# Optimization experiments

Hardware: AMD Instinct MI355X
Metric: run time of the kernel (lower is better)

The kernel has to match this reference:

```python
import jax, jax.numpy as jnp
import numpy as np
from jax import lax

# --- STE quantizers matching the torch autograd.Functions ---
@jax.custom_vjp
def binary_quantize_w(x):
    return jnp.sign(x)

def _bqw_fwd(x):
    return jnp.sign(x), None

def _bqw_bwd(_, g):
    return (g,)  # straight-through identity

binary_quantize_w.defvjp(_bqw_fwd, _bqw_bwd)

@jax.custom_vjp
def binary_quantize_a(x):
    return jnp.sign(x)

def _bqa_fwd(x):
    return jnp.sign(x), x

def _bqa_bwd(x, g):
    return (jnp.clip(2.0 - jnp.abs(2.0 * x), a_min=0.0) * g,)

binary_quantize_a.defvjp(_bqa_fwd, _bqa_bwd)

STRIDE = 1
PAD = 1

def setup_inputs() -> dict:
    key = jax.random.key(0)
    k1, k2, k3 = jax.random.split(key, 3)
    x = jax.random.normal(k1, (32, 256, 56, 56), dtype=jnp.float32)
    M = jax.random.normal(k2, (256, 256, 3, 3), dtype=jnp.float32)
    Alpha = jax.random.uniform(k3, (256, 1, 1), dtype=jnp.float32)
    return {"x": x, "M": M, "Alpha": Alpha}

def reference(x, M, Alpha):
    bw = binary_quantize_w(M)        # (O, I, kh, kw), +/-1
    ba = binary_quantize_a(x)        # (N, C, H, W), +/-1
    out = lax.conv_general_dilated(
        ba, bw,
        window_strides=(STRIDE, STRIDE),
        padding=[(PAD, PAD), (PAD, PAD)],
        dimension_numbers=("NCHW", "OIHW", "NCHW"),
    )
    # Alpha (O,1,1) broadcasts over (N, O, H, W) trailing dims -> per-channel scale
    return out * Alpha
```

## Files before the change

kernel.cpp:

```cpp
#include <hip/hip_runtime.h>
#include <stdint.h>


typedef __attribute__((ext_vector_type(16))) float floatx16;
typedef __attribute__((ext_vector_type(8)))  int   intx8;

#define N_IMG 32
#define C_IN  256
#define O_OUT 256
#define HP 58
#define WP 58
#define GPI 3136
#define APAD_POS ((size_t)N_IMG * HP * WP)
#define ROWB 128
#define APAD_BYTES (APAD_POS * ROWB)
#define TPI 13
#define AL_CHUNKS 536
#define WL_CHUNKS 768
#define WROW 8192
#define WPK_STEP (3 * WROW)

__device__ __forceinline__ unsigned int sgn4(float x) {
    return x > 0.f ? 0x2u : (x < 0.f ? 0xAu : 0u);
}

__device__ __forceinline__ void glds16(const unsigned char* g, unsigned char* l) {
    __builtin_amdgcn_global_load_lds(
        (const __attribute__((address_space(1))) unsigned int*)g,
        (__attribute__((address_space(3))) unsigned int*)l, 16, 0, 0);
}

__device__ __forceinline__ unsigned int nib16(unsigned int w) {
    return (w & 0xFu) | ((w >> 4) & 0xF0u) |
           ((w >> 8) & 0xF00u) | ((w >> 12) & 0xF000u);
}
__device__ __forceinline__ unsigned int nibc(unsigned int lo, unsigned int hi) {
    return nib16(lo) | (nib16(hi) << 16);
}

__global__ __launch_bounds__(256) void binarize_act(
    const float* __restrict__ x, unsigned char* __restrict__ apad)
{
    int bid = blockIdx.x;
    int n = bid / HP;
    int hp = bid - n * HP;
    int tid = threadIdx.x;

    unsigned char* rowp = apad + (size_t)(n * HP + hp) * WP * ROWB;
    uint4 z = {0u, 0u, 0u, 0u};

    if (hp == 0 || hp == HP - 1) {
#pragma unroll
        for (int j = 0; j < 2; ++j) {
            int t = tid + 256 * j;
            if (t < WP * 8) {
                int w = t >> 3, g = t & 7;
                *(uint4*)(rowp + (size_t)w * ROWB + g * 16) = z;
            }
        }
        return;
    }
    int h = hp - 1;

    __shared__ unsigned int tile[C_IN * 15];
    __shared__ unsigned int lds2[56 * 65];

    const float* xb = x + ((size_t)n * C_IN) * GPI + h * 56;
#pragma unroll
    for (int j = 0; j < 14; ++j) {
        int t = tid + 256 * j;
        int ci = t / 14;
        int w4 = t - ci * 14;
        float4 v = *(const float4*)(xb + (size_t)ci * GPI + w4 * 4);
        tile[ci * 15 + w4] = sgn4(v.x) | (sgn4(v.y) << 8) |
                             (sgn4(v.z) << 16) | (sgn4(v.w) << 24);
    }
    __syncthreads();

#pragma unroll
    for (int j = 0; j < 14; ++j) {
        int t = tid + 256 * j;
        int wlo = t & 3;
        int cq  = (t >> 2) & 63;
        int whi = t >> 8;
        int sh = wlo * 8;
        unsigned int r = 0;
#pragma unroll
        for (int i = 0; i < 4; ++i) {
            unsigned int v = tile[(cq * 4 + i) * 15 + whi];
            r |= ((v >> sh) & 0xFFu) << (8 * i);
        }
        lds2[(whi * 4 + wlo) * 65 + cq] = r;
    }
    __syncthreads();

#pragma unroll
    for (int j = 0; j < 2; ++j) {
        int t = tid + 256 * j;
        if (t < 448) {
            int w = t >> 3, g = t & 7;
            uint4 a = *(uint4*)&lds2[w * 65 + g * 8];
            uint4 b = *(uint4*)&lds2[w * 65 + g * 8 + 4];
            uint4 v;
            v.x = nibc(a.x, a.y);
            v.y = nibc(a.z, a.w);
            v.z = nibc(b.x, b.y);
            v.w = nibc(b.z, b.w);
            *(uint4*)(rowp + (size_t)(w + 1) * ROWB + g * 16) = v;
        }
    }
    if (tid < 16) {
        int g = tid & 7;
        int col = (tid >> 3) * (WP - 1);
        *(uint4*)(rowp + (size_t)col * ROWB + g * 16) = z;
    }
}

__global__ __launch_bounds__(64) void pack_w(
    const float* __restrict__ M, unsigned char* __restrict__ wpk)
{
    int gid = blockIdx.x * 64 + threadIdx.x;
    int o = gid >> 6;
    int c4 = (gid & 63) << 2;
    int c0q = c4 >> 6;
    int half = (c4 & 63) >> 1;
    const float* mb = M + (size_t)(o * C_IN + c4) * 9;
#pragma unroll
    for (int t = 0; t < 9; ++t) {
        int kh = t / 3, kw = t - 3 * (t / 3);
        unsigned int r = sgn4(mb[t]) | (sgn4(mb[9 + t]) << 4) |
                         (sgn4(mb[18 + t]) << 8) | (sgn4(mb[27 + t]) << 12);
        size_t dst = (size_t)((kh * 4 + c0q) * 3 + kw) * WROW + o * 32 + half;
        *(unsigned short*)(wpk + dst) = (unsigned short)r;
    }
}

__global__ __launch_bounds__(256, 2) void bconv_gemm(
    const unsigned char* __restrict__ apad,
    const unsigned char* __restrict__ wpk,
    const float* __restrict__ alpha,
    float* __restrict__ out)
{
    __shared__ __align__(16) unsigned char Al[AL_CHUNKS * 16];
    __shared__ __align__(16) unsigned char Wl[WL_CHUNKS * 16];

    const int tid = threadIdx.x;
    const int wv = tid >> 6, lane = tid & 63;
    const int l31 = lane & 31, hb = lane >> 5;

    const int hw = blockIdx.x;
    const int bid = (hw & 7) * 104 + (hw >> 3);

    const int img = bid / 26;
    const int rem = bid - img * 26;
    const int tl = rem >> 1, ot = rem & 1;
    const int g0 = tl << 8;
    const int h0 = g0 / 56, w0 = g0 - h0 * 56;
    const int o_base = ot << 7;
    const int Q0 = (img * HP + h0) * WP + w0;

    int al_pos[3], al_co[3], al_dst[3], al_on[3];
#pragma unroll
    for (int it = 0; it < 3; ++it) {
        int g = (it < 2) ? (tid + (it << 8)) : (512 + tid);
        al_on[it] = (it < 2) || (tid < AL_CHUNKS - 512);
        int pos = g >> 1;
        al_pos[it] = pos;
        al_co[it]  = (((g & 1) ^ ((pos >> 2) & 1)) << 4);
        al_dst[it] = g << 4;
    }
    int wl_src[3], wl_dst[3];
#pragma unroll
    for (int it = 0; it < 3; ++it) {
        int g = tid + (it << 8);
        int r = g >> 1, q = (g & 1) ^ ((r >> 2) & 1);
        int kw = r >> 7, ol = r & 127;
        wl_src[it] = kw * WROW + (o_base + ol) * 32 + (q << 4);
        wl_dst[it] = g << 4;
    }

    const int o_half  = (wv >> 1) << 6;
    const int px_half = (wv & 1) << 7;

    int pos_tab[4], pxg[4];
#pragma unroll
    for (int nt = 0; nt < 4; ++nt) {
        int px = px_half + (nt << 5) + l31;
        pxg[nt] = g0 + px;
        int pxc = (pxg[nt] < GPI) ? px : (GPI - 1 - g0);
        pos_tab[nt] = pxc + 2 * ((w0 + pxc) / 56);
    }

    floatx16 acc[2][4] = {};
    const uint4 z4 = {0u, 0u, 0u, 0u};

    for (int t = 0; t < 12; ++t) {
        const int kh = t >> 2;
        const int cb0 = (t & 3) << 5;
        const int rowbase = Q0 + kh * WP;
        const int plim = (int)APAD_POS - 1 - rowbase;
        const unsigned char* asrc = apad + ((size_t)rowbase * ROWB + cb0);
        const unsigned char* wsrc = wpk + (size_t)t * WPK_STEP;

        __syncthreads();
#pragma unroll
        for (int it = 0; it < 3; ++it) {
            if (al_on[it]) {
                int p = al_pos[it] < plim ? al_pos[it] : plim;
                glds16(asrc + (size_t)p * ROWB + al_co[it], &Al[al_dst[it]]);
            }
        }
#pragma unroll
        for (int it = 0; it < 3; ++it)
            glds16(wsrc + wl_src[it], &Wl[wl_dst[it]]);
        __syncthreads();

#pragma unroll
        for (int kw = 0; kw < 3; ++kw) {
            union F { uint4 q[2]; intx8 v; };
            F af[2];
#pragma unroll
            for (int mt = 0; mt < 2; ++mt) {
                int rl = (kw << 7) + o_half + (mt << 5) + l31;
                int L = (rl << 1) + (hb ^ ((rl >> 2) & 1));
                af[mt].q[0] = *(const uint4*)&Wl[(size_t)L << 4];
                af[mt].q[1] = z4;
            }
#pragma unroll
            for (int nt = 0; nt < 4; ++nt) {
                int pos = pos_tab[nt] + kw;
                int L = (pos << 1) + (hb ^ ((pos >> 2) & 1));
                F bf;
                bf.q[0] = *(const uint4*)&Al[(size_t)L << 4];
                bf.q[1] = z4;
#pragma unroll
                for (int mt = 0; mt < 2; ++mt)
                    acc[mt][nt] = __builtin_amdgcn_mfma_scale_f32_32x32x64_f8f6f4(
                        af[mt].v, bf.v, acc[mt][nt],
                        4, 4,
                        0, 0x7F7F7F7F,
                        0, 0x7F7F7F7F);
            }
        }
    }

#pragma unroll
    for (int mt = 0; mt < 2; ++mt) {
#pragma unroll
        for (int r = 0; r < 16; ++r) {
            int o_loc = o_half + (mt << 5) + (r & 3) + ((r >> 2) << 3) + (hb << 2);
            int o_g = o_base + o_loc;
            float a = alpha[o_g];
            float* ob = out + ((size_t)(img * O_OUT + o_g)) * GPI;
#pragma unroll
            for (int nt = 0; nt < 4; ++nt) {
                if (pxg[nt] < GPI) ob[pxg[nt]] = acc[mt][nt][r] * a;
            }
        }
    }
}

extern "C" void kernel_launch(void* const* d_in, const int* in_sizes, int n_in,
                              void* d_out, int out_size, void* d_ws, size_t ws_size,
                              hipStream_t stream) {
    const float* x     = (const float*)d_in[0];
    const float* M     = (const float*)d_in[1];
    const float* alpha = (const float*)d_in[2];
    float* out = (float*)d_out;

    unsigned char* apad = (unsigned char*)d_ws;
    unsigned char* wpk  = apad + APAD_BYTES;

    binarize_act<<<dim3(N_IMG * HP), dim3(256), 0, stream>>>(x, apad);
    pack_w<<<dim3(256), dim3(64), 0, stream>>>(M, wpk);
    bconv_gemm<<<dim3(N_IMG * TPI * 2), dim3(256), 0, stream>>>(apad, wpk, alpha, out);
}
```

Baseline: 243.2 us.

## Double-buffer activation tiles in LDS and load weights directly from global

The GEMM main loop is restructured from 12 stages of 32 bytes each into 6 stages of 64 channel-bytes each. Activation tiles are double-buffered in LDS, so the next stage's global-to-LDS copy is issued before computing on the current one, and the second barrier per stage goes away. Weight fragments are no longer staged in LDS and are read straight from global memory (likely L2 hits) into registers. This cuts synchronisation and LDS traffic but adds global-load latency for the weights on the critical path and more register pressure.

```diff
diff --git a/kernel.cpp b/kernel.cpp
--- a/kernel.cpp
+++ b/kernel.cpp
@@ -15,8 +15,8 @@
 #define ROWB 128
 #define APAD_BYTES (APAD_POS * ROWB)
 #define TPI 13
-#define AL_CHUNKS 536
-#define WL_CHUNKS 768
+#define NPOS 268
+#define AL_HALF (NPOS * 64)
 #define WROW 8192
 #define WPK_STEP (3 * WROW)
 
@@ -135,14 +135,28 @@
     }
 }
 
+__device__ __forceinline__ void stage_half(const unsigned char* __restrict__ src,
+    int plim, int tid, unsigned char* dst)
+{
+#pragma unroll
+    for (int it = 0; it < 5; ++it) {
+        int g = tid + (it << 8);
+        if (it < 4 || tid < 48) {
+            int pos = g >> 2;
+            int jj = (g & 3) ^ (pos & 3);
+            int p = pos < plim ? pos : plim;
+            glds16(src + (size_t)p * ROWB + (jj << 4), dst + ((size_t)g << 4));
+        }
+    }
+}
+
 __global__ __launch_bounds__(256, 2) void bconv_gemm(
     const unsigned char* __restrict__ apad,
     const unsigned char* __restrict__ wpk,
     const float* __restrict__ alpha,
     float* __restrict__ out)
 {
-    __shared__ __align__(16) unsigned char Al[AL_CHUNKS * 16];
-    __shared__ __align__(16) unsigned char Wl[WL_CHUNKS * 16];
+    __shared__ __align__(16) unsigned char Al[2][AL_HALF];
 
     const int tid = threadIdx.x;
     const int wv = tid >> 6, lane = tid & 63;
@@ -159,26 +173,6 @@
     const int o_base = ot << 7;
     const int Q0 = (img * HP + h0) * WP + w0;
 
-    int al_pos[3], al_co[3], al_dst[3], al_on[3];
-#pragma unroll
-    for (int it = 0; it < 3; ++it) {
-        int g = (it < 2) ? (tid + (it << 8)) : (512 + tid);
-        al_on[it] = (it < 2) || (tid < AL_CHUNKS - 512);
-        int pos = g >> 1;
-        al_pos[it] = pos;
-        al_co[it]  = (((g & 1) ^ ((pos >> 2) & 1)) << 4);
-        al_dst[it] = g << 4;
-    }
-    int wl_src[3], wl_dst[3];
-#pragma unroll
-    for (int it = 0; it < 3; ++it) {
-        int g = tid + (it << 8);
-        int r = g >> 1, q = (g & 1) ^ ((r >> 2) & 1);
-        int kw = r >> 7, ol = r & 127;
-        wl_src[it] = kw * WROW + (o_base + ol) * 32 + (q << 4);
-        wl_dst[it] = g << 4;
-    }
-
     const int o_half  = (wv >> 1) << 6;
     const int px_half = (wv & 1) << 7;
 
@@ -194,52 +188,53 @@
     floatx16 acc[2][4] = {};
     const uint4 z4 = {0u, 0u, 0u, 0u};
 
-    for (int t = 0; t < 12; ++t) {
-        const int kh = t >> 2;
-        const int cb0 = (t & 3) << 5;
-        const int rowbase = Q0 + kh * WP;
-        const int plim = (int)APAD_POS - 1 - rowbase;
-        const unsigned char* asrc = apad + ((size_t)rowbase * ROWB + cb0);
-        const unsigned char* wsrc = wpk + (size_t)t * WPK_STEP;
+    stage_half(apad + (size_t)Q0 * ROWB, (int)APAD_POS - 1 - Q0, tid, &Al[0][0]);
+
+    for (int s = 0; s < 6; ++s) {
+        const int kh = s >> 1, ch2 = s & 1;
 
         __syncthreads();
-#pragma unroll
-        for (int it = 0; it < 3; ++it) {
-            if (al_on[it]) {
-                int p = al_pos[it] < plim ? al_pos[it] : plim;
-                glds16(asrc + (size_t)p * ROWB + al_co[it], &Al[al_dst[it]]);
-            }
-        }
-#pragma unroll
-        for (int it = 0; it < 3; ++it)
-            glds16(wsrc + wl_src[it], &Wl[wl_dst[it]]);
-        __syncthreads();
-
-#pragma unroll
-        for (int kw = 0; kw < 3; ++kw) {
+
+        if (s < 5) {
+            const int s1 = s + 1;
+            const int rb1 = Q0 + (s1 >> 1) * WP;
+            stage_half(apad + ((size_t)rb1 * ROWB + (size_t)(s1 & 1) * 64),
+                       (int)APAD_POS - 1 - rb1, tid, &Al[s1 & 1][0]);
+        }
+
+        const unsigned char* AlC = &Al[s & 1][0];
+#pragma unroll
+        for (int cc = 0; cc < 2; ++cc) {
+            const int c0q = (ch2 << 1) + cc;
             union F { uint4 q[2]; intx8 v; };
-            F af[2];
-#pragma unroll
-            for (int mt = 0; mt < 2; ++mt) {
-                int rl = (kw << 7) + o_half + (mt << 5) + l31;
-                int L = (rl << 1) + (hb ^ ((rl >> 2) & 1));
-                af[mt].q[0] = *(const uint4*)&Wl[(size_t)L << 4];
-                af[mt].q[1] = z4;
-            }
-#pragma unroll
-            for (int nt = 0; nt < 4; ++nt) {
-                int pos = pos_tab[nt] + kw;
-                int L = (pos << 1) + (hb ^ ((pos >> 2) & 1));
-                F bf;
-                bf.q[0] = *(const uint4*)&Al[(size_t)L << 4];
-                bf.q[1] = z4;
-#pragma unroll
-                for (int mt = 0; mt < 2; ++mt)
-                    acc[mt][nt] = __builtin_amdgcn_mfma_scale_f32_32x32x64_f8f6f4(
-                        af[mt].v, bf.v, acc[mt][nt],
-                        4, 4,
-                        0, 0x7F7F7F7F,
-                        0, 0x7F7F7F7F);
+            F wf[2][3];
+            const unsigned char* wb = wpk +
+                (size_t)((kh * 4 + c0q) * 3) * WROW +
+                (size_t)(o_base + o_half + l31) * 32 + (hb << 4);
+#pragma unroll
+            for (int mt = 0; mt < 2; ++mt)
+#pragma unroll
+                for (int kw = 0; kw < 3; ++kw) {
+                    wf[mt][kw].q[0] = *(const uint4*)(wb + (size_t)kw * WROW + (size_t)mt * 1024);
+                    wf[mt][kw].q[1] = z4;
+                }
+            const int ch = (cc << 1) | hb;
+#pragma unroll
+            for (int kw = 0; kw < 3; ++kw) {
+#pragma unroll
+                for (int nt = 0; nt < 4; ++nt) {
+                    int pk = pos_tab[nt] + kw;
+                    F bf;
+                    bf.q[0] = *(const uint4*)&AlC[(size_t)(pk << 6) + ((ch ^ (pk & 3)) << 4)];
+                    bf.q[1] = z4;
+#pragma unroll
+                    for (int mt = 0; mt < 2; ++mt)
+                        acc[mt][nt] = __builtin_amdgcn_mfma_scale_f32_32x32x64_f8f6f4(
+                            wf[mt][kw].v, bf.v, acc[mt][nt],
+                            4, 4,
+                            0, 0x7F7F7F7F,
+                            0, 0x7F7F7F7F);
+                }
             }
         }
     }
```

Measured after the change: 501.0 us. 106% more time.
